# Optimization experiments

Hardware: AMD Instinct MI355X
Metric: run time of the kernel (lower is better)

## Reference

```python
import jax, jax.numpy as jnp
import numpy as np

B, M, N, L = 8, 384, 1536, 20  # batch, checks (detectors), error mechanisms, BP layers
ROW_W = 8  # check-node degree of sparse parity-check matrix H


def setup_inputs() -> dict:
    key = jax.random.key(0)
    ks = jax.random.split(key, 10)
    # Sparse binary check matrix: each row has exactly ROW_W ones (LDPC-like DEM).
    rng = np.random.default_rng(0)
    H_np = np.zeros((M, N), np.float32)
    for i in range(M):
        H_np[i, rng.choice(N, ROW_W, replace=False)] = 1.0
    H = jnp.asarray(H_np)
    llrs = jax.random.uniform(ks[0], (N,), minval=0.5, maxval=2.0)
    syndromes = jax.random.randint(ks[1], (B, M, 1), 0, 2).astype(jnp.float32)
    errors = jax.random.randint(ks[2], (B, N), 0, 2).astype(jnp.float32)
    # Per-layer learned weights (damped so 20 BP iterations stay numerically stable).
    weights_de = jax.random.uniform(ks[3], (L, M, N), minval=0.1, maxval=0.25)
    weights_llr = jax.random.uniform(ks[4], (L, N), minval=0.5, maxval=1.0)
    marg_weights_de = jax.random.uniform(ks[5], (M, N), minval=0.5, maxval=1.0)
    marg_weights_llr = jax.random.uniform(ks[6], (N,), minval=0.5, maxval=1.0)
    residual_weights = jax.random.uniform(ks[7], (L,), minval=0.0, maxval=0.1)
    rhos = jnp.ones((L,), jnp.float32) / L  # init: ones normalized by layers
    return dict(syndromes=syndromes, errors=errors, H=H, llrs=llrs,
                weights_de=weights_de, weights_llr=weights_llr,
                marg_weights_de=marg_weights_de, marg_weights_llr=marg_weights_llr,
                residual_weights=residual_weights, rhos=rhos)


def reference(syndromes, errors, H, llrs, weights_de, weights_llr,
              marg_weights_de, marg_weights_llr, residual_weights, rhos):
    sign = (1.0 - 2.0 * syndromes) * H          # (B,M,N): (-1)^syndrome masked by H
    one_minus_e = 1.0 - errors                  # (B,N)

    def step(msg_dn, per_layer):
        w_de, w_llr, res_w, rho = per_layer
        # --- error (variable) node update ---
        base = H * (llrs * w_llr)                                     # (M,N)
        msg_en = (base + jnp.sum(msg_dn * w_de, axis=1, keepdims=True)) * H - msg_dn
        # --- detector (check) node update: tanh-product with self-exclusion by division ---
        d = jnp.tanh(msg_en * 0.5)
        d = jnp.where(d == 0.0, 1.0, d)
        p = jnp.prod(d, axis=2, keepdims=True)                        # (B,M,1)
        msg_dn_new = 2.0 * jnp.arctanh(p / d) * sign + res_w * msg_dn
        # --- marginals (beliefs) + per-layer loss ---
        beliefs = jnp.sum(msg_dn_new * marg_weights_de, axis=1) + llrs * marg_weights_llr  # (B,N)
        loss_b = jnp.sum(jax.nn.softplus(beliefs) - one_minus_e * beliefs, axis=1) * rho   # (B,)
        return msg_dn_new, loss_b

    msg0 = jnp.zeros((syndromes.shape[0], H.shape[0], H.shape[1]), jnp.float32)
    _, losses = jax.lax.scan(step, msg0, (weights_de, weights_llr, residual_weights, rhos))
    return jnp.sum(losses) / syndromes.shape[0]  # scalar mean-over-batch loss
```

## Files before the change

kernel.cpp:

```cpp
#include <hip/hip_runtime.h>
#include <math.h>

#define MB 8
#define MM 384
#define NN 1536
#define LL 20
#define RW 8
#define HE 4
#define NE (MM*RW)
#define NT 768
#define VP 12
#define VG 3

#define SOFT_BAR() asm volatile("s_waitcnt lgkmcnt(0)\n\ts_barrier" ::: "memory")

__global__ __launch_bounds__(256) void setup_kernel(
    const float* __restrict__ H,
    const float* __restrict__ llrs,
    const float* __restrict__ w_llr,
    const float* __restrict__ w_de,
    const float* __restrict__ marg_de,
    int*   __restrict__ col_pack,
    float* __restrict__ base_e,
    float* __restrict__ wde_vT,
    float* __restrict__ marg_vT,
    int*   __restrict__ gcnt,
    float* __restrict__ out) {
    const int m = blockIdx.x;
    const int t = threadIdx.x;
    const int w = t >> 6, lane = t & 63;
    __shared__ int s_qcol[4][RW];
    __shared__ int s_qcnt[4];
    __shared__ int s_col[RW];
    __shared__ int s_pos[RW];

    const float* row = H + (size_t)m * NN;
    int count = 0;
    for (int c0 = w * 384; c0 < (w + 1) * 384; c0 += 64) {
        float v = row[c0 + lane];
        unsigned long long mask = __ballot(v != 0.0f);
        if (v != 0.0f) {
            int pos = count + (int)__popcll(mask & ((1ull << lane) - 1ull));
            if (pos < RW) s_qcol[w][pos] = c0 + lane;
        }
        count += (int)__popcll(mask);
    }
    if (lane == 0) s_qcnt[w] = (count < RW) ? count : RW;
    __syncthreads();
    if (t == 0) {
        int off = 0;
        for (int q = 0; q < 4; ++q)
            for (int i = 0; i < s_qcnt[q]; ++i) {
                if (off < RW) s_col[off] = s_qcol[q][i];
                ++off;
            }
    }
    __syncthreads();

    if (t < RW) {
        int c = s_col[t];
        int pos = atomicAdd(&gcnt[c], 1);
        if (pos >= VP) pos = VP - 1;
        s_pos[t] = pos;
        col_pack[m * RW + t] = c | (pos << 16);
        marg_vT[((pos >> 2) * NN + c) * 4 + (pos & 3)] = marg_de[m * NN + c];
    }
    if (m == 0 && t == 0) out[0] = 0.0f;
    __syncthreads();

    for (int idx = t; idx < LL * RW; idx += 256) {
        int l = idx >> 3;
        int k = idx & 7;
        int c = s_col[k];
        int pos = s_pos[k];
        wde_vT[((l * VG + (pos >> 2)) * NN + c) * 4 + (pos & 3)] =
            w_de[(size_t)l * MM * NN + (size_t)m * NN + c];
        base_e[l * NE + m * RW + k] = llrs[c] * w_llr[l * NN + c];
    }
}

#define LAYER_BODY(lv, WC0, WC1, BC, WN0, WN1, BN)                            \
{                                                                             \
               \
    {                                                                         \
        int lb = ((lv) + 1 < LL) ? ((lv) + 1) : (LL - 1);                     \
        _Pragma("unroll")                                                     \
        for (int jg = 0; jg < VG; ++jg) {                                     \
            float4 a = ((const float4*)wde_vT)[(lb * VG + jg) * NN + t];      \
            WN0[jg*4+0]=a.x; WN0[jg*4+1]=a.y; WN0[jg*4+2]=a.z; WN0[jg*4+3]=a.w; \
            float4 c4 = ((const float4*)wde_vT)[(lb * VG + jg) * NN + t + NT];\
            WN1[jg*4+0]=c4.x; WN1[jg*4+1]=c4.y; WN1[jg*4+2]=c4.z; WN1[jg*4+3]=c4.w; \
        }                                                                     \
        const float4 bp4 = ((const float4*)(base_e_g + lb * NE))[t];          \
        BN[0]=bp4.x; BN[1]=bp4.y; BN[2]=bp4.z; BN[3]=bp4.w;                   \
    }                                                                         \
            \
    {                                                                         \
        float S0 = 0.0f, S1 = 0.0f, bel0 = bias[0], bel1 = bias[1];           \
        _Pragma("unroll")                                                     \
        for (int jg = 0; jg < VG; ++jg) {                                     \
            float4 a = ((const float4*)s_cN)[jg * NN + t];                    \
            S0   += a.x*WC0[jg*4+0] + a.y*WC0[jg*4+1] + a.z*WC0[jg*4+2] + a.w*WC0[jg*4+3]; \
            bel0 += a.x*mg0[jg*4+0] + a.y*mg0[jg*4+1] + a.z*mg0[jg*4+2] + a.w*mg0[jg*4+3]; \
            float4 c4 = ((const float4*)s_cN)[jg * NN + t + NT];              \
            S1   += c4.x*WC1[jg*4+0] + c4.y*WC1[jg*4+1] + c4.z*WC1[jg*4+2] + c4.w*WC1[jg*4+3]; \
            bel1 += c4.x*mg1[jg*4+0] + c4.y*mg1[jg*4+1] + c4.z*mg1[jg*4+2] + c4.w*mg1[jg*4+3]; \
        }                                                                     \
        s_S[t]      = S0;                                                     \
        s_S[t + NT] = S1;                                                     \
        if ((lv) > 0) {                                                       \
            const float rr = s_rho[(lv) - 1];                                 \
            float sp0 = fmaxf(bel0, 0.0f) + __logf(1.0f + __expf(-fabsf(bel0))); \
            float sp1 = fmaxf(bel1, 0.0f) + __logf(1.0f + __expf(-fabsf(bel1))); \
            loss += rr * ((sp0 - omeg[0] * bel0) + (sp1 - omeg[1] * bel1));   \
        }                                                                     \
    }                                                                         \
    SOFT_BAR();                \
    {                                                                         \
        const float rw_ = s_rw[(lv)];                                         \
        float d[HE];                                                          \
        _Pragma("unroll")                                                     \
        for (int k = 0; k < HE; ++k) {                                        \
            float te = BC[k] + s_S[col[k]] - msg[k];                          \
            float e  = __expf(te);                                            \
            float dd = 1.0f - 2.0f * __builtin_amdgcn_rcpf(e + 1.0f);         \
            dd = fminf(fmaxf(dd, -1.0f), 1.0f);                               \
            if (dd == 0.0f) dd = 1.0f;                                        \
            d[k] = dd;                                                        \
        }                                                                     \
        float pre2 = d[0] * d[1];                                             \
        float suf1 = d[2] * d[3];                                             \
        float p4   = pre2 * suf1;                                             \
        float pot  = __shfl_xor(p4, 1, 64);                                   \
        float ex[HE];                                                         \
        ex[0] = d[1] * suf1;                                                  \
        ex[1] = d[0] * suf1;                                                  \
        ex[2] = pre2 * d[3];                                                  \
        ex[3] = pre2 * d[2];                                                  \
        _Pragma("unroll")                                                     \
        for (int k = 0; k < HE; ++k) {                                        \
            float x  = ex[k] * pot;                                           \
            float r  = (1.0f + x) * __builtin_amdgcn_rcpf(1.0f - x);          \
            float nm = sgn * __logf(r) + rw_ * msg[k];                        \
            msg[k] = nm;                                                      \
            s_cN[esl[k]] = nm;                                                \
        }                                                                     \
    }                                                                         \
    SOFT_BAR();                  \
}

__global__ __launch_bounds__(NT) void bp_kernel(
    const float* __restrict__ synd,
    const float* __restrict__ errors,
    const float* __restrict__ llrs,
    const float* __restrict__ marg_llr,
    const float* __restrict__ res_w,
    const float* __restrict__ rhos,
    const int*   __restrict__ col_pack,
    const float* __restrict__ base_e_g,
    const float* __restrict__ wde_vT,
    const float* __restrict__ marg_vT,
    float* __restrict__ out) {

    __shared__ float s_cN[NN * VP];
    __shared__ float s_S[NN];
    __shared__ float s_rw[LL];
    __shared__ float s_rho[LL];
    __shared__ float s_red[12];

    const int b = blockIdx.x;
    const int t = threadIdx.x;
    const int m = t >> 1;

    int col[HE], esl[HE];
    {
        const int4 cp = ((const int4*)col_pack)[t];
        int v[HE] = {cp.x, cp.y, cp.z, cp.w};
        #pragma unroll
        for (int k = 0; k < HE; ++k) {
            int c = v[k] & 0xFFFF, pos = v[k] >> 16;
            col[k] = c;
            esl[k] = ((pos >> 2) * NN + c) * 4 + (pos & 3);
        }
    }
    float msg[HE] = {0.0f, 0.0f, 0.0f, 0.0f};
    const float sgn = 1.0f - 2.0f * synd[b * MM + m];

    float bias[2], omeg[2];
    #pragma unroll
    for (int i = 0; i < 2; ++i) {
        int n = t + i * NT;
        bias[i] = llrs[n] * marg_llr[n];
        omeg[i] = 1.0f - errors[b * NN + n];
    }

    float mg0[VP], mg1[VP];
    #pragma unroll
    for (int jg = 0; jg < VG; ++jg) {
        float4 a = ((const float4*)marg_vT)[jg * NN + t];
        mg0[jg*4+0] = a.x; mg0[jg*4+1] = a.y; mg0[jg*4+2] = a.z; mg0[jg*4+3] = a.w;
        float4 c4 = ((const float4*)marg_vT)[jg * NN + t + NT];
        mg1[jg*4+0] = c4.x; mg1[jg*4+1] = c4.y; mg1[jg*4+2] = c4.z; mg1[jg*4+3] = c4.w;
    }
    float wcA0[VP], wcA1[VP], wcB0[VP], wcB1[VP];
    #pragma unroll
    for (int jg = 0; jg < VG; ++jg) {
        float4 a = ((const float4*)wde_vT)[jg * NN + t];
        wcA0[jg*4+0] = a.x; wcA0[jg*4+1] = a.y; wcA0[jg*4+2] = a.z; wcA0[jg*4+3] = a.w;
        float4 c4 = ((const float4*)wde_vT)[jg * NN + t + NT];
        wcA1[jg*4+0] = c4.x; wcA1[jg*4+1] = c4.y; wcA1[jg*4+2] = c4.z; wcA1[jg*4+3] = c4.w;
    }
    float bcA[HE], bcB[HE];
    {
        const float4 bp4 = ((const float4*)base_e_g)[t];
        bcA[0] = bp4.x; bcA[1] = bp4.y; bcA[2] = bp4.z; bcA[3] = bp4.w;
    }

    #pragma unroll
    for (int j = 0; j < 6; ++j)
        ((float4*)s_cN)[j * NT + t] = make_float4(0.f, 0.f, 0.f, 0.f);
    if (t < LL) { s_rw[t] = res_w[t]; s_rho[t] = rhos[t]; }

    float loss = 0.0f;
    __syncthreads();

    for (int l = 0; l < LL; l += 2) {
        LAYER_BODY(l,     wcA0, wcA1, bcA, wcB0, wcB1, bcB);
        LAYER_BODY(l + 1, wcB0, wcB1, bcB, wcA0, wcA1, bcA);
    }

    {
        const float rr = s_rho[LL - 1];
        float bel0 = bias[0], bel1 = bias[1];
        #pragma unroll
        for (int jg = 0; jg < VG; ++jg) {
            float4 a = ((const float4*)s_cN)[jg * NN + t];
            bel0 += a.x*mg0[jg*4+0] + a.y*mg0[jg*4+1] + a.z*mg0[jg*4+2] + a.w*mg0[jg*4+3];
            float4 c4 = ((const float4*)s_cN)[jg * NN + t + NT];
            bel1 += c4.x*mg1[jg*4+0] + c4.y*mg1[jg*4+1] + c4.z*mg1[jg*4+2] + c4.w*mg1[jg*4+3];
        }
        float sp0 = fmaxf(bel0, 0.0f) + __logf(1.0f + __expf(-fabsf(bel0)));
        float sp1 = fmaxf(bel1, 0.0f) + __logf(1.0f + __expf(-fabsf(bel1)));
        loss += rr * ((sp0 - omeg[0] * bel0) + (sp1 - omeg[1] * bel1));
    }

    #pragma unroll
    for (int off = 32; off > 0; off >>= 1)
        loss += __shfl_down(loss, off, 64);
    int wave = t >> 6, lane = t & 63;
    if (lane == 0) s_red[wave] = loss;
    __syncthreads();
    if (t == 0) {
        float tot = 0.0f;
        #pragma unroll
        for (int w = 0; w < 12; ++w) tot += s_red[w];
        atomicAdd(out, tot * (1.0f / (float)MB));
    }
}

extern "C" void kernel_launch(void* const* d_in, const int* in_sizes, int n_in,
                              void* d_out, int out_size, void* d_ws, size_t ws_size,
                              hipStream_t stream) {
    const float* synd     = (const float*)d_in[0];
    const float* errors   = (const float*)d_in[1];
    const float* H        = (const float*)d_in[2];
    const float* llrs     = (const float*)d_in[3];
    const float* w_de     = (const float*)d_in[4];
    const float* w_llr    = (const float*)d_in[5];
    const float* marg_de  = (const float*)d_in[6];
    const float* marg_llr = (const float*)d_in[7];
    const float* res_w    = (const float*)d_in[8];
    const float* rhos     = (const float*)d_in[9];
    float* out = (float*)d_out;

    float* wde_vT  = (float*)d_ws;
    float* marg_vT = wde_vT + (size_t)LL * VG * NN * 4;
    int*   gcnt    = (int*)(marg_vT + VG * NN * 4);
    float* base_e  = (float*)(gcnt + NN);
    int*   col_pack= (int*)(base_e + (size_t)LL * NE);

    hipMemsetAsync(gcnt, 0, NN * sizeof(int), stream);
    setup_kernel<<<MM, 256, 0, stream>>>(H, llrs, w_llr, w_de, marg_de,
                                         col_pack, base_e, wde_vT, marg_vT,
                                         gcnt, out);
    bp_kernel<<<MB, NT, 0, stream>>>(synd, errors, llrs, marg_llr, res_w, rhos,
                                     col_pack, base_e, wde_vT, marg_vT, out);
}
```

Measured before the change: 143.7 us.

## Replace per-column gather with LDS atomic scatter of weighted messages, one barrier per layer

Check-to-variable messages are no longer stored in a per-column slot table and reduced by gathering 12 slots per column. Each edge now scatters msg*w_de for the next layer and msg*marg into triple-buffered LDS accumulators using shared-memory atomicAdd. This removes the hipMemset and the slot-assignment atomics in setup, drops the large per-thread weight register arrays, and cuts the layer body from two barriers to one. In exchange it relies on LDS float atomics, which may contend on columns with many incident edges, and on triple-buffer rotation being correct.

```diff
diff --git a/kernel.cpp b/kernel.cpp
--- a/kernel.cpp
+++ b/kernel.cpp
@@ -9,8 +9,6 @@
 #define HE 4
 #define NE (MM*RW)
 #define NT 768
-#define VP 12
-#define VG 3
 
 #define SOFT_BAR() asm volatile("s_waitcnt lgkmcnt(0)\n\ts_barrier" ::: "memory")
 
@@ -22,9 +20,8 @@
     const float* __restrict__ marg_de,
     int*   __restrict__ col_pack,
     float* __restrict__ base_e,
-    float* __restrict__ wde_vT,
-    float* __restrict__ marg_vT,
-    int*   __restrict__ gcnt,
+    float* __restrict__ wde_e,
+    float* __restrict__ marg_e,
     float* __restrict__ out) {
     const int m = blockIdx.x;
     const int t = threadIdx.x;
@@ -32,7 +29,6 @@
     __shared__ int s_qcol[4][RW];
     __shared__ int s_qcnt[4];
     __shared__ int s_col[RW];
-    __shared__ int s_pos[RW];
 
     const float* row = H + (size_t)m * NN;
     int count = 0;
@@ -59,94 +55,77 @@
 
     if (t < RW) {
         int c = s_col[t];
-        int pos = atomicAdd(&gcnt[c], 1);
-        if (pos >= VP) pos = VP - 1;
-        s_pos[t] = pos;
-        col_pack[m * RW + t] = c | (pos << 16);
-        marg_vT[((pos >> 2) * NN + c) * 4 + (pos & 3)] = marg_de[m * NN + c];
+        col_pack[m * RW + t] = c;
+        marg_e[m * RW + t] = marg_de[m * NN + c];
     }
     if (m == 0 && t == 0) out[0] = 0.0f;
-    __syncthreads();
 
     for (int idx = t; idx < LL * RW; idx += 256) {
         int l = idx >> 3;
         int k = idx & 7;
         int c = s_col[k];
-        int pos = s_pos[k];
-        wde_vT[((l * VG + (pos >> 2)) * NN + c) * 4 + (pos & 3)] =
-            w_de[(size_t)l * MM * NN + (size_t)m * NN + c];
+        wde_e[l * NE + m * RW + k]  = w_de[(size_t)l * MM * NN + (size_t)m * NN + c];
         base_e[l * NE + m * RW + k] = llrs[c] * w_llr[l * NN + c];
     }
 }
 
-#define LAYER_BODY(lv, WC0, WC1, BC, WN0, WN1, BN)                            \
+#define LAYER(lv, IR, IW, II, WC, WN, BC, BN)                                 \
 {                                                                             \
-               \
+    if ((lv) + 2 < LL) {                                                      \
+        const float4 w4 = ((const float4*)(wde_e + ((lv) + 2) * NE))[t];      \
+        WN[0] = w4.x; WN[1] = w4.y; WN[2] = w4.z; WN[3] = w4.w;               \
+    }                                                                         \
     {                                                                         \
-        int lb = ((lv) + 1 < LL) ? ((lv) + 1) : (LL - 1);                     \
-        _Pragma("unroll")                                                     \
-        for (int jg = 0; jg < VG; ++jg) {                                     \
-            float4 a = ((const float4*)wde_vT)[(lb * VG + jg) * NN + t];      \
-            WN0[jg*4+0]=a.x; WN0[jg*4+1]=a.y; WN0[jg*4+2]=a.z; WN0[jg*4+3]=a.w; \
-            float4 c4 = ((const float4*)wde_vT)[(lb * VG + jg) * NN + t + NT];\
-            WN1[jg*4+0]=c4.x; WN1[jg*4+1]=c4.y; WN1[jg*4+2]=c4.z; WN1[jg*4+3]=c4.w; \
-        }                                                                     \
-        const float4 bp4 = ((const float4*)(base_e_g + lb * NE))[t];          \
-        BN[0]=bp4.x; BN[1]=bp4.y; BN[2]=bp4.z; BN[3]=bp4.w;                   \
-    }                                                                         \
-            \
+        const int lb = ((lv) + 1 < LL) ? (lv) + 1 : (LL - 1);                 \
+        const float4 b4 = ((const float4*)(base_e + lb * NE))[t];             \
+        BN[0] = b4.x; BN[1] = b4.y; BN[2] = b4.z; BN[3] = b4.w;               \
+    }                                                                         \
+    float d_[HE];                                                             \
+    _Pragma("unroll")                                                         \
+    for (int k = 0; k < HE; ++k) {                                            \
+        float te = BC[k] + s_S[IR][col[k]] - msg[k];                          \
+        float e  = __expf(te);                                                \
+        float dd = 1.0f - 2.0f * __builtin_amdgcn_rcpf(e + 1.0f);             \
+        dd = fminf(fmaxf(dd, -1.0f), 1.0f);                                   \
+        if (dd == 0.0f) dd = 1.0f;                                            \
+        d_[k] = dd;                                                           \
+    }                                                                         \
     {                                                                         \
-        float S0 = 0.0f, S1 = 0.0f, bel0 = bias[0], bel1 = bias[1];           \
-        _Pragma("unroll")                                                     \
-        for (int jg = 0; jg < VG; ++jg) {                                     \
-            float4 a = ((const float4*)s_cN)[jg * NN + t];                    \
-            S0   += a.x*WC0[jg*4+0] + a.y*WC0[jg*4+1] + a.z*WC0[jg*4+2] + a.w*WC0[jg*4+3]; \
-            bel0 += a.x*mg0[jg*4+0] + a.y*mg0[jg*4+1] + a.z*mg0[jg*4+2] + a.w*mg0[jg*4+3]; \
-            float4 c4 = ((const float4*)s_cN)[jg * NN + t + NT];              \
-            S1   += c4.x*WC1[jg*4+0] + c4.y*WC1[jg*4+1] + c4.z*WC1[jg*4+2] + c4.w*WC1[jg*4+3]; \
-            bel1 += c4.x*mg1[jg*4+0] + c4.y*mg1[jg*4+1] + c4.z*mg1[jg*4+2] + c4.w*mg1[jg*4+3]; \
-        }                                                                     \
-        s_S[t]      = S0;                                                     \
-        s_S[t + NT] = S1;                                                     \
-        if ((lv) > 0) {                                                       \
-            const float rr = s_rho[(lv) - 1];                                 \
-            float sp0 = fmaxf(bel0, 0.0f) + __logf(1.0f + __expf(-fabsf(bel0))); \
-            float sp1 = fmaxf(bel1, 0.0f) + __logf(1.0f + __expf(-fabsf(bel1))); \
-            loss += rr * ((sp0 - omeg[0] * bel0) + (sp1 - omeg[1] * bel1));   \
-        }                                                                     \
-    }                                                                         \
-    SOFT_BAR();                \
-    {                                                                         \
-        const float rw_ = s_rw[(lv)];                                         \
-        float d[HE];                                                          \
-        _Pragma("unroll")                                                     \
-        for (int k = 0; k < HE; ++k) {                                        \
-            float te = BC[k] + s_S[col[k]] - msg[k];                          \
-            float e  = __expf(te);                                            \
-            float dd = 1.0f - 2.0f * __builtin_amdgcn_rcpf(e + 1.0f);         \
-            dd = fminf(fmaxf(dd, -1.0f), 1.0f);                               \
-            if (dd == 0.0f) dd = 1.0f;                                        \
-            d[k] = dd;                                                        \
-        }                                                                     \
-        float pre2 = d[0] * d[1];                                             \
-        float suf1 = d[2] * d[3];                                             \
+        float pre2 = d_[0] * d_[1];                                           \
+        float suf1 = d_[2] * d_[3];                                           \
         float p4   = pre2 * suf1;                                             \
         float pot  = __shfl_xor(p4, 1, 64);                                   \
         float ex[HE];                                                         \
-        ex[0] = d[1] * suf1;                                                  \
-        ex[1] = d[0] * suf1;                                                  \
-        ex[2] = pre2 * d[3];                                                  \
-        ex[3] = pre2 * d[2];                                                  \
+        ex[0] = d_[1] * suf1;                                                 \
+        ex[1] = d_[0] * suf1;                                                 \
+        ex[2] = pre2 * d_[3];                                                 \
+        ex[3] = pre2 * d_[2];                                                 \
+        const float rw_ = s_rw[(lv)];                                         \
         _Pragma("unroll")                                                     \
         for (int k = 0; k < HE; ++k) {                                        \
             float x  = ex[k] * pot;                                           \
             float r  = (1.0f + x) * __builtin_amdgcn_rcpf(1.0f - x);          \
-            float nm = sgn * __logf(r) + rw_ * msg[k];                        \
-            msg[k] = nm;                                                      \
-            s_cN[esl[k]] = nm;                                                \
+            msg[k] = sgn * __logf(r) + rw_ * msg[k];                          \
         }                                                                     \
     }                                                                         \
-    SOFT_BAR();                  \
+    if ((lv) + 1 < LL) {                                                      \
+        _Pragma("unroll")                                                     \
+        for (int k = 0; k < HE; ++k)                                          \
+            atomicAdd(&s_S[IW][col[k]], msg[k] * WC[k]);                      \
+    }                                                                         \
+    _Pragma("unroll")                                                         \
+    for (int k = 0; k < HE; ++k)                                              \
+        atomicAdd(&s_B[IW][col[k]], msg[k] * me[k]);                          \
+    if ((lv) + 2 < LL) { s_S[II][n0] = 0.0f;  s_S[II][n1] = 0.0f;  }          \
+    if ((lv) + 1 < LL) { s_B[II][n0] = bias0; s_B[II][n1] = bias1; }          \
+    if ((lv) > 0) {                                                           \
+        const float rr = s_rho[(lv) > 0 ? (lv) - 1 : 0];                      \
+        float bel0 = s_B[IR][n0], bel1 = s_B[IR][n1];                         \
+        float sp0 = fmaxf(bel0, 0.0f) + __logf(1.0f + __expf(-fabsf(bel0)));  \
+        float sp1 = fmaxf(bel1, 0.0f) + __logf(1.0f + __expf(-fabsf(bel1)));  \
+        loss += rr * ((sp0 - om0 * bel0) + (sp1 - om1 * bel1));               \
+    }                                                                         \
+    SOFT_BAR();                                                               \
 }
 
 __global__ __launch_bounds__(NT) void bp_kernel(
@@ -157,13 +136,13 @@
     const float* __restrict__ res_w,
     const float* __restrict__ rhos,
     const int*   __restrict__ col_pack,
-    const float* __restrict__ base_e_g,
-    const float* __restrict__ wde_vT,
-    const float* __restrict__ marg_vT,
+    const float* __restrict__ base_e,
+    const float* __restrict__ wde_e,
+    const float* __restrict__ marg_e,
     float* __restrict__ out) {
 
-    __shared__ float s_cN[NN * VP];
-    __shared__ float s_S[NN];
+    __shared__ float s_S[3][NN];
+    __shared__ float s_B[3][NN];
     __shared__ float s_rw[LL];
     __shared__ float s_rho[LL];
     __shared__ float s_red[12];
@@ -172,76 +151,69 @@
     const int t = threadIdx.x;
     const int m = t >> 1;
 
-    int col[HE], esl[HE];
+    int col[HE];
     {
         const int4 cp = ((const int4*)col_pack)[t];
-        int v[HE] = {cp.x, cp.y, cp.z, cp.w};
-        #pragma unroll
-        for (int k = 0; k < HE; ++k) {
-            int c = v[k] & 0xFFFF, pos = v[k] >> 16;
-            col[k] = c;
-            esl[k] = ((pos >> 2) * NN + c) * 4 + (pos & 3);
-        }
+        col[0] = cp.x; col[1] = cp.y; col[2] = cp.z; col[3] = cp.w;
+    }
+    float me[HE];
+    {
+        const float4 m4 = ((const float4*)marg_e)[t];
+        me[0] = m4.x; me[1] = m4.y; me[2] = m4.z; me[3] = m4.w;
     }
     float msg[HE] = {0.0f, 0.0f, 0.0f, 0.0f};
     const float sgn = 1.0f - 2.0f * synd[b * MM + m];
 
-    float bias[2], omeg[2];
-    #pragma unroll
-    for (int i = 0; i < 2; ++i) {
-        int n = t + i * NT;
-        bias[i] = llrs[n] * marg_llr[n];
-        omeg[i] = 1.0f - errors[b * NN + n];
-    }
-
-    float mg0[VP], mg1[VP];
-    #pragma unroll
-    for (int jg = 0; jg < VG; ++jg) {
-        float4 a = ((const float4*)marg_vT)[jg * NN + t];
-        mg0[jg*4+0] = a.x; mg0[jg*4+1] = a.y; mg0[jg*4+2] = a.z; mg0[jg*4+3] = a.w;
-        float4 c4 = ((const float4*)marg_vT)[jg * NN + t + NT];
-        mg1[jg*4+0] = c4.x; mg1[jg*4+1] = c4.y; mg1[jg*4+2] = c4.z; mg1[jg*4+3] = c4.w;
-    }
-    float wcA0[VP], wcA1[VP], wcB0[VP], wcB1[VP];
-    #pragma unroll
-    for (int jg = 0; jg < VG; ++jg) {
-        float4 a = ((const float4*)wde_vT)[jg * NN + t];
-        wcA0[jg*4+0] = a.x; wcA0[jg*4+1] = a.y; wcA0[jg*4+2] = a.z; wcA0[jg*4+3] = a.w;
-        float4 c4 = ((const float4*)wde_vT)[jg * NN + t + NT];
-        wcA1[jg*4+0] = c4.x; wcA1[jg*4+1] = c4.y; wcA1[jg*4+2] = c4.z; wcA1[jg*4+3] = c4.w;
-    }
-    float bcA[HE], bcB[HE];
-    {
-        const float4 bp4 = ((const float4*)base_e_g)[t];
-        bcA[0] = bp4.x; bcA[1] = bp4.y; bcA[2] = bp4.z; bcA[3] = bp4.w;
-    }
-
-    #pragma unroll
-    for (int j = 0; j < 6; ++j)
-        ((float4*)s_cN)[j * NT + t] = make_float4(0.f, 0.f, 0.f, 0.f);
+    const int n0 = t, n1 = t + NT;
+    const float bias0 = llrs[n0] * marg_llr[n0];
+    const float bias1 = llrs[n1] * marg_llr[n1];
+    const float om0 = 1.0f - errors[b * NN + n0];
+    const float om1 = 1.0f - errors[b * NN + n1];
+
     if (t < LL) { s_rw[t] = res_w[t]; s_rho[t] = rhos[t]; }
 
+    s_S[0][n0] = 0.0f;  s_S[0][n1] = 0.0f;
+    s_S[1][n0] = 0.0f;  s_S[1][n1] = 0.0f;
+    s_B[1][n0] = bias0; s_B[1][n1] = bias1;
+
+    float wA[HE] = {0,0,0,0}, wB[HE] = {0,0,0,0};
+    float bcA[HE], bcB[HE] = {0,0,0,0};
+    {
+        const float4 w4 = ((const float4*)(wde_e + 1 * NE))[t];
+        wA[0] = w4.x; wA[1] = w4.y; wA[2] = w4.z; wA[3] = w4.w;
+        const float4 b4 = ((const float4*)base_e)[t];
+        bcA[0] = b4.x; bcA[1] = b4.y; bcA[2] = b4.z; bcA[3] = b4.w;
+    }
     float loss = 0.0f;
     __syncthreads();
 
-    for (int l = 0; l < LL; l += 2) {
-        LAYER_BODY(l,     wcA0, wcA1, bcA, wcB0, wcB1, bcB);
-        LAYER_BODY(l + 1, wcB0, wcB1, bcB, wcA0, wcA1, bcA);
-    }
+    LAYER(0,  0, 1, 2, wA, wB, bcA, bcB)
+    LAYER(1,  1, 2, 0, wB, wA, bcB, bcA)
+    LAYER(2,  2, 0, 1, wA, wB, bcA, bcB)
+    LAYER(3,  0, 1, 2, wB, wA, bcB, bcA)
+    LAYER(4,  1, 2, 0, wA, wB, bcA, bcB)
+    LAYER(5,  2, 0, 1, wB, wA, bcB, bcA)
+    LAYER(6,  0, 1, 2, wA, wB, bcA, bcB)
+    LAYER(7,  1, 2, 0, wB, wA, bcB, bcA)
+    LAYER(8,  2, 0, 1, wA, wB, bcA, bcB)
+    LAYER(9,  0, 1, 2, wB, wA, bcB, bcA)
+    LAYER(10, 1, 2, 0, wA, wB, bcA, bcB)
+    LAYER(11, 2, 0, 1, wB, wA, bcB, bcA)
+    LAYER(12, 0, 1, 2, wA, wB, bcA, bcB)
+    LAYER(13, 1, 2, 0, wB, wA, bcB, bcA)
+    LAYER(14, 2, 0, 1, wA, wB, bcA, bcB)
+    LAYER(15, 0, 1, 2, wB, wA, bcB, bcA)
+    LAYER(16, 1, 2, 0, wA, wB, bcA, bcB)
+    LAYER(17, 2, 0, 1, wB, wA, bcB, bcA)
+    LAYER(18, 0, 1, 2, wA, wB, bcA, bcB)
+    LAYER(19, 1, 2, 0, wB, wA, bcB, bcA)
 
     {
         const float rr = s_rho[LL - 1];
-        float bel0 = bias[0], bel1 = bias[1];
-        #pragma unroll
-        for (int jg = 0; jg < VG; ++jg) {
-            float4 a = ((const float4*)s_cN)[jg * NN + t];
-            bel0 += a.x*mg0[jg*4+0] + a.y*mg0[jg*4+1] + a.z*mg0[jg*4+2] + a.w*mg0[jg*4+3];
-            float4 c4 = ((const float4*)s_cN)[jg * NN + t + NT];
-            bel1 += c4.x*mg1[jg*4+0] + c4.y*mg1[jg*4+1] + c4.z*mg1[jg*4+2] + c4.w*mg1[jg*4+3];
-        }
+        float bel0 = s_B[2][n0], bel1 = s_B[2][n1];
         float sp0 = fmaxf(bel0, 0.0f) + __logf(1.0f + __expf(-fabsf(bel0)));
         float sp1 = fmaxf(bel1, 0.0f) + __logf(1.0f + __expf(-fabsf(bel1)));
-        loss += rr * ((sp0 - omeg[0] * bel0) + (sp1 - omeg[1] * bel1));
+        loss += rr * ((sp0 - om0 * bel0) + (sp1 - om1 * bel1));
     }
 
     #pragma unroll
@@ -273,16 +245,13 @@
     const float* rhos     = (const float*)d_in[9];
     float* out = (float*)d_out;
 
-    float* wde_vT  = (float*)d_ws;
-    float* marg_vT = wde_vT + (size_t)LL * VG * NN * 4;
-    int*   gcnt    = (int*)(marg_vT + VG * NN * 4);
-    float* base_e  = (float*)(gcnt + NN);
-    int*   col_pack= (int*)(base_e + (size_t)LL * NE);
-
-    hipMemsetAsync(gcnt, 0, NN * sizeof(int), stream);
+    float* wde_e   = (float*)d_ws;
+    float* base_e  = wde_e + (size_t)LL * NE;
+    float* marg_e  = base_e + (size_t)LL * NE;
+    int*   col_pack= (int*)(marg_e + NE);
+
     setup_kernel<<<MM, 256, 0, stream>>>(H, llrs, w_llr, w_de, marg_de,
-                                         col_pack, base_e, wde_vT, marg_vT,
-                                         gcnt, out);
+                                         col_pack, base_e, wde_e, marg_e, out);
     bp_kernel<<<MB, NT, 0, stream>>>(synd, errors, llrs, marg_llr, res_w, rhos,
-                                     col_pack, base_e, wde_vT, marg_vT, out);
-}
+                                     col_pack, base_e, wde_e, marg_e, out);
+}
```

After: 269.8 us. 87.8% more time.
